# Kernel optimization log

Measured on AMD Instinct MI355X. Metric: run time of the kernel, lower is better.

## Reference

```python
import jax, jax.numpy as jnp
import numpy as np

B, S, D, H = 4, 2048, 1024, 16
HD = D // H  # head dim = 64


def setup_inputs() -> dict:
    key = jax.random.key(0)
    ks = jax.random.split(key, 6)
    scale = D ** -0.5
    x = jax.random.normal(ks[0], (B, S, D), dtype=jnp.float32)
    # per-head q/k/v projections stacked: [H, D, HD] (bias-free, as in GPT Head)
    Wq = jax.random.normal(ks[1], (H, D, HD), dtype=jnp.float32) * scale
    Wk = jax.random.normal(ks[2], (H, D, HD), dtype=jnp.float32) * scale
    Wv = jax.random.normal(ks[3], (H, D, HD), dtype=jnp.float32) * scale
    # output projection Linear(D, D) with bias
    Wp = jax.random.normal(ks[4], (D, D), dtype=jnp.float32) * scale
    bp = jax.random.normal(ks[5], (D,), dtype=jnp.float32) * 0.01
    return {"x": x, "Wq": Wq, "Wk": Wk, "Wv": Wv, "Wp": Wp, "bp": bp}


def reference(x, Wq, Wk, Wv, Wp, bp):
    # q,k,v: [B, H, S, HD]
    q = jnp.einsum("bsd,hdk->bhsk", x, Wq)
    k = jnp.einsum("bsd,hdk->bhsk", x, Wk)
    v = jnp.einsum("bsd,hdk->bhsk", x, Wv)
    scale = HD ** -0.5
    # attention scores [B, H, S, S] with causal mask
    scores = jnp.einsum("bhsk,bhtk->bhst", q, k) * scale
    causal = jnp.tril(jnp.ones((S, S), dtype=bool))
    scores = jnp.where(causal, scores, jnp.finfo(scores.dtype).min)
    att = jax.nn.softmax(scores, axis=-1)
    out = jnp.einsum("bhst,bhtk->bhsk", att, v)  # [B, H, S, HD]
    # concat heads -> [B, S, D], then output projection
    out = out.transpose(0, 2, 1, 3).reshape(B, S, D)
    return out @ Wp + bp
```

## Files before the change

kernel.cpp:

```cpp
#include <hip/hip_runtime.h>
#include <stdint.h>

#define B_  4
#define S_  2048
#define D_  1024
#define H_  16
#define HD_ 64

typedef __attribute__((ext_vector_type(8))) short bf16x8;
typedef __attribute__((ext_vector_type(4))) short bf16x4;
typedef __attribute__((ext_vector_type(4))) float f32x4;

#define MFMA32(a, b, c) __builtin_amdgcn_mfma_f32_16x16x32_bf16(a, b, c, 0, 0, 0)

__device__ __forceinline__ unsigned short f2bf(float f) {
  union { float f; uint32_t u; } cv; cv.f = f;
  uint32_t x = cv.u;
  uint32_t r = (x + 0x7fffu + ((x >> 16) & 1u)) >> 16;
  return (unsigned short)r;
}

__device__ __forceinline__ unsigned short f2bf_rz(float f) {
  union { float f; uint32_t u; } cv; cv.f = f;
  return (unsigned short)(cv.u >> 16);
}

__device__ __forceinline__ void gload_lds16(const unsigned short* g, unsigned short* l) {
  __builtin_amdgcn_global_load_lds((const __attribute__((address_space(1))) void*)g,
                                   (__attribute__((address_space(3))) void*)l, 16, 0, 0);
}

__global__ void k_cast_x(const float* __restrict__ x, unsigned short* __restrict__ xb) {
  size_t i = ((size_t)blockIdx.x * 256 + threadIdx.x) * 8;
  float4 a = *(const float4*)(x + i);
  float4 b = *(const float4*)(x + i + 4);
  bf16x8 o;
  o[0] = (short)f2bf(a.x); o[1] = (short)f2bf(a.y);
  o[2] = (short)f2bf(a.z); o[3] = (short)f2bf(a.w);
  o[4] = (short)f2bf(b.x); o[5] = (short)f2bf(b.y);
  o[6] = (short)f2bf(b.z); o[7] = (short)f2bf(b.w);
  *(bf16x8*)(xb + i) = o;
}

__global__ void k_wqkv_t(const float* __restrict__ Wq, const float* __restrict__ Wk,
                         const float* __restrict__ Wv, unsigned short* __restrict__ W1T) {
  __shared__ unsigned short tile[64][65];
  const float* W = (blockIdx.z == 0) ? Wq : (blockIdx.z == 1) ? Wk : Wv;
  int h = blockIdx.y;
  int d0 = blockIdx.x * 64;
  int tx = threadIdx.x & 63;
  int tg = threadIdx.x >> 6;
  const float* src = W + (size_t)h * (D_ * HD_) + (size_t)d0 * HD_;
#pragma unroll
  for (int r = 0; r < 16; ++r) {
    int dy = tg * 16 + r;
    tile[tx][dy] = f2bf(src[(size_t)dy * HD_ + tx]);
  }
  __syncthreads();
  unsigned short* dst = W1T + ((size_t)blockIdx.z * 1024 + (size_t)h * 64) * 1024 + d0;
#pragma unroll
  for (int r = 0; r < 16; ++r) {
    int hd = tg * 16 + r;
    dst[(size_t)hd * 1024 + tx] = tile[hd][tx];
  }
}

__global__ void k_wp_t(const float* __restrict__ Wp, unsigned short* __restrict__ WpT) {
  __shared__ unsigned short tile[64][65];
  int n0 = blockIdx.x * 64, k0 = blockIdx.y * 64;
  int tx = threadIdx.x & 63;
  int tg = threadIdx.x >> 6;
#pragma unroll
  for (int r = 0; r < 16; ++r) {
    int ky = tg * 16 + r;
    tile[tx][ky] = f2bf(Wp[(size_t)(k0 + ky) * D_ + n0 + tx]);
  }
  __syncthreads();
#pragma unroll
  for (int r = 0; r < 16; ++r) {
    int ny = tg * 16 + r;
    WpT[(size_t)(n0 + ny) * D_ + k0 + tx] = tile[ny][tx];
  }
}

__global__ __launch_bounds__(256) void k_gemm_qkv(const unsigned short* __restrict__ xb,
                                                  const unsigned short* __restrict__ W1T,
                                                  unsigned short* __restrict__ qb,
                                                  unsigned short* __restrict__ kb,
                                                  unsigned short* __restrict__ vt) {
  __shared__ __align__(16) unsigned short lds[128 * 136];
  unsigned short* As = lds;
  unsigned short* Bs = lds + 4096;
  const int K = 1024;
  int tid = threadIdx.x;
  int lane = tid & 63;
  int w = tid >> 6;
  int c = lane & 15, g = lane >> 4;
  int wr = w >> 1, wc = w & 1;
  int nwg = gridDim.x * gridDim.y;
  int bid = blockIdx.y * gridDim.x + blockIdx.x;
  int swzb = (bid & 7) * (nwg >> 3) + (bid >> 3);
  int bx = swzb % gridDim.x, by = swzb / gridDim.x;
  int m0 = by * 128;
  int n0 = bx * 128;
  f32x4 acc[4][4];
#pragma unroll
  for (int m = 0; m < 4; ++m)
#pragma unroll
    for (int n = 0; n < 4; ++n) acc[m][n] = (f32x4){0.f, 0.f, 0.f, 0.f};

  int t0 = tid, t1 = tid + 256;
  const unsigned short* ga0 = xb + (size_t)(m0 + (t0 >> 2)) * K + 8 * (t0 & 3);
  const unsigned short* ga1 = xb + (size_t)(m0 + (t1 >> 2)) * K + 8 * (t1 & 3);
  const unsigned short* gb0 = W1T + (size_t)(n0 + (t0 >> 2)) * K + 8 * (t0 & 3);
  const unsigned short* gb1 = W1T + (size_t)(n0 + (t1 >> 2)) * K + 8 * (t1 & 3);

  for (int kk = 0; kk < K; kk += 32) {
    __syncthreads();
    gload_lds16(ga0 + kk, &As[t0 * 8]);
    gload_lds16(ga1 + kk, &As[t1 * 8]);
    gload_lds16(gb0 + kk, &Bs[t0 * 8]);
    gload_lds16(gb1 + kk, &Bs[t1 * 8]);
    __syncthreads();
    bf16x8 af[4], bfr[4];
#pragma unroll
    for (int m = 0; m < 4; ++m)
      af[m] = *(const bf16x8*)&As[(wr * 64 + m * 16 + c) * 32 + 8 * g];
#pragma unroll
    for (int n = 0; n < 4; ++n)
      bfr[n] = *(const bf16x8*)&Bs[(wc * 64 + n * 16 + c) * 32 + 8 * g];
#pragma unroll
    for (int m = 0; m < 4; ++m)
#pragma unroll
      for (int n = 0; n < 4; ++n) acc[m][n] = MFMA32(af[m], bfr[n], acc[m][n]);
  }

  int qkv = n0 >> 10;
  int b = m0 >> 11;
  int s0 = m0 & 2047;
  if (qkv < 2) {
    unsigned short* dst = (qkv == 0) ? qb : kb;
    float sc = (qkv == 0) ? 0.125f : 1.0f;
#pragma unroll
    for (int m = 0; m < 4; ++m)
#pragma unroll
      for (int n = 0; n < 4; ++n)
#pragma unroll
        for (int r = 0; r < 4; ++r) {
          int s = s0 + wr * 64 + m * 16 + 4 * g + r;
          int Cn = n0 + wc * 64 + n * 16 + c;
          int h = (Cn >> 6) & 15;
          int hd = Cn & 63;
          dst[((size_t)(b * 16 + h) * S_ + s) * HD_ + hd] = f2bf(acc[m][n][r] * sc);
        }
  } else {
    __syncthreads();
#pragma unroll
    for (int m = 0; m < 4; ++m)
#pragma unroll
      for (int n = 0; n < 4; ++n) {
        int col = wc * 64 + n * 16 + c;
        int row4 = wr * 64 + m * 16 + 4 * g;
        bf16x4 pk;
        pk[0] = (short)f2bf(acc[m][n][0]);
        pk[1] = (short)f2bf(acc[m][n][1]);
        pk[2] = (short)f2bf(acc[m][n][2]);
        pk[3] = (short)f2bf(acc[m][n][3]);
        *(bf16x4*)&lds[col * 136 + row4] = pk;
      }
    __syncthreads();
    int col = tid >> 1;
    int sh = (tid & 1) * 64;
    int Cn = n0 + col;
    int h = (Cn >> 6) & 15;
    int hd = Cn & 63;
    unsigned short* dst = vt + ((size_t)(b * 16 + h) * HD_ + hd) * S_ + s0 + sh;
#pragma unroll
    for (int j = 0; j < 8; ++j)
      *(bf16x8*)(dst + 8 * j) = *(const bf16x8*)&lds[col * 136 + sh + 8 * j];
  }
}

__device__ __forceinline__ void stage_kv(const unsigned short* kp, const unsigned short* vp,
                                         int tb, unsigned short* Ks, unsigned short* Vs,
                                         int tid) {
  int i0 = tid, i1 = tid + 256;
  int r0 = i0 >> 3, ch0 = ((i0 & 7) ^ (r0 & 7)) << 3;
  int r1 = i1 >> 3, ch1 = ((i1 & 7) ^ (r1 & 7)) << 3;
  gload_lds16(kp + (size_t)(tb + r0) * HD_ + ch0, &Ks[i0 * 8]);
  gload_lds16(kp + (size_t)(tb + r1) * HD_ + ch1, &Ks[i1 * 8]);
  gload_lds16(vp + (size_t)r0 * S_ + tb + ch0, &Vs[i0 * 8]);
  gload_lds16(vp + (size_t)r1 * S_ + tb + ch1, &Vs[i1 * 8]);
}

__global__ __launch_bounds__(256) void k_attn(const unsigned short* __restrict__ qb,
                                              const unsigned short* __restrict__ kb,
                                              const unsigned short* __restrict__ vt,
                                              unsigned short* __restrict__ attn) {
  __shared__ __align__(16) unsigned short Ks[2][64 * 64];
  __shared__ __align__(16) unsigned short Vs[2][64 * 64];
  int tid = threadIdx.x;
  int lane = tid & 63;
  int w = tid >> 6;
  int c = lane & 15, g = lane >> 4;
  int swz = ((blockIdx.x & 7) << 6) | (blockIdx.x >> 3);
  int bh = swz >> 3;
  int pr = swz & 7;
  const unsigned short* kp = kb + (size_t)bh * S_ * HD_;
  const unsigned short* vp = vt + (size_t)bh * HD_ * S_;
  int b = bh >> 4, h = bh & 15;

  for (int p = 0; p < 2; ++p) {
    int j = p ? (15 - pr) : pr;
    int q0w = j * 128 + w * 32;
    const unsigned short* qp = qb + ((size_t)bh * S_ + q0w) * HD_;
    bf16x8 qf[2][2];
#pragma unroll
    for (int qs = 0; qs < 2; ++qs)
#pragma unroll
      for (int h2 = 0; h2 < 2; ++h2)
        qf[qs][h2] = *(const bf16x8*)(qp + (size_t)(qs * 16 + c) * HD_ + h2 * 32 + 8 * g);

    const f32x4 fz = {0.f, 0.f, 0.f, 0.f};
    f32x4 oacc[4][2];
#pragma unroll
    for (int c4 = 0; c4 < 4; ++c4)
#pragma unroll
      for (int qs = 0; qs < 2; ++qs) oacc[c4][qs] = fz;
    float m[2] = {-1e30f, -1e30f};
    float l[2] = {0.f, 0.f};

    int nkb = 2 * j + 2;
    int nkw = (q0w + 95) >> 6;

    stage_kv(kp, vp, 0, Ks[0], Vs[0], tid);
    __syncthreads();

    for (int kt = 0; kt < nkb; ++kt) {
      int cur = kt & 1;
      if (kt + 1 < nkb) stage_kv(kp, vp, (kt + 1) << 6, Ks[cur ^ 1], Vs[cur ^ 1], tid);
      if (kt < nkw) {
        int tb = kt << 6;
        const unsigned short* KsC = Ks[cur];
        const unsigned short* VsC = Vs[cur];
        f32x4 st[4][2];
#pragma unroll
        for (int k4 = 0; k4 < 4; ++k4) {
          int row = k4 * 16 + c;
          int rx = row & 7;
          bf16x8 a0 = *(const bf16x8*)&KsC[row * 64 + ((g ^ rx) << 3)];
          bf16x8 a1 = *(const bf16x8*)&KsC[row * 64 + (((4 + g) ^ rx) << 3)];
#pragma unroll
          for (int qs = 0; qs < 2; ++qs) {
            f32x4 t0 = MFMA32(a0, qf[qs][0], fz);
            st[k4][qs] = MFMA32(a1, qf[qs][1], t0);
          }
        }
        if (tb + 63 > q0w) {
#pragma unroll
          for (int k4 = 0; k4 < 4; ++k4)
#pragma unroll
            for (int qs = 0; qs < 2; ++qs)
#pragma unroll
              for (int r = 0; r < 4; ++r)
                if (tb + k4 * 16 + 4 * g + r > q0w + qs * 16 + c) st[k4][qs][r] = -1e30f;
        }
        bf16x8 pa[2][2];
#pragma unroll
        for (int qs = 0; qs < 2; ++qs) {
          float mx = -1e30f;
#pragma unroll
          for (int k4 = 0; k4 < 4; ++k4)
#pragma unroll
            for (int r = 0; r < 4; ++r) mx = fmaxf(mx, st[k4][qs][r]);
          mx = fmaxf(mx, __shfl_xor(mx, 16));
          mx = fmaxf(mx, __shfl_xor(mx, 32));
          if (!__all(mx - m[qs] <= 8.f)) {
            float m_new = fmaxf(m[qs], mx);
            float resc = __expf(m[qs] - m_new);
            m[qs] = m_new;
            float rb0 = __shfl(resc, 4 * g + 0);
            float rb1 = __shfl(resc, 4 * g + 1);
            float rb2 = __shfl(resc, 4 * g + 2);
            float rb3 = __shfl(resc, 4 * g + 3);
#pragma unroll
            for (int c4 = 0; c4 < 4; ++c4) {
              oacc[c4][qs][0] *= rb0; oacc[c4][qs][1] *= rb1;
              oacc[c4][qs][2] *= rb2; oacc[c4][qs][3] *= rb3;
            }
            l[qs] *= resc;
          }
          float mh = m[qs];
          float rs = 0.f;
#pragma unroll
          for (int k4 = 0; k4 < 4; ++k4)
#pragma unroll
            for (int r = 0; r < 4; ++r) {
              float e = __expf(st[k4][qs][r] - mh);
              st[k4][qs][r] = e;
              rs += e;
            }
          rs += __shfl_xor(rs, 16);
          rs += __shfl_xor(rs, 32);
          l[qs] += rs;
#pragma unroll
          for (int ks = 0; ks < 2; ++ks)
#pragma unroll
            for (int jj = 0; jj < 8; ++jj)
              pa[qs][ks][jj] = (short)f2bf_rz(st[ks * 2 + (jj >> 2)][qs][jj & 3]);
        }
#pragma unroll
        for (int c4 = 0; c4 < 4; ++c4) {
          int row = c4 * 16 + c;
          int rx = row & 7;
#pragma unroll
          for (int ks = 0; ks < 2; ++ks) {
            int e0 = ks * 32 + 4 * g;
            int e1 = e0 + 16;
            int s0 = (((e0 >> 3) ^ rx) << 3) | (e0 & 7);
            int s1 = (((e1 >> 3) ^ rx) << 3) | (e1 & 7);
            bf16x4 v0 = *(const bf16x4*)&VsC[row * 64 + s0];
            bf16x4 v1 = *(const bf16x4*)&VsC[row * 64 + s1];
            bf16x8 vf;
            vf[0] = v0[0]; vf[1] = v0[1]; vf[2] = v0[2]; vf[3] = v0[3];
            vf[4] = v1[0]; vf[5] = v1[1]; vf[6] = v1[2]; vf[7] = v1[3];
#pragma unroll
            for (int qs = 0; qs < 2; ++qs)
              oacc[c4][qs] = MFMA32(pa[qs][ks], vf, oacc[c4][qs]);
          }
        }
      }
      __syncthreads();
    }
#pragma unroll
    for (int qs = 0; qs < 2; ++qs) {
      float linv = 1.f / l[qs];
      float lb0 = __shfl(linv, 4 * g + 0);
      float lb1 = __shfl(linv, 4 * g + 1);
      float lb2 = __shfl(linv, 4 * g + 2);
      float lb3 = __shfl(linv, 4 * g + 3);
      float lb[4] = {lb0, lb1, lb2, lb3};
      unsigned short* op = attn + ((size_t)b * S_ + q0w + qs * 16) * D_ + h * HD_;
#pragma unroll
      for (int c4 = 0; c4 < 4; ++c4)
#pragma unroll
        for (int r = 0; r < 4; ++r)
          op[(size_t)(4 * g + r) * D_ + c4 * 16 + c] = f2bf(oacc[c4][qs][r] * lb[r]);
    }
  }
}

__global__ __launch_bounds__(256) void k_gemm_out(const unsigned short* __restrict__ at,
                                                  const unsigned short* __restrict__ WpT,
                                                  const float* __restrict__ bp,
                                                  float* __restrict__ out) {
  __shared__ __align__(16) unsigned short As[128 * 32];
  __shared__ __align__(16) unsigned short Bs[128 * 32];
  const int K = 1024;
  int tid = threadIdx.x;
  int lane = tid & 63;
  int w = tid >> 6;
  int c = lane & 15, g = lane >> 4;
  int wr = w >> 1, wc = w & 1;
  int nwg = gridDim.x * gridDim.y;
  int bid = blockIdx.y * gridDim.x + blockIdx.x;
  int swzb = (bid & 7) * (nwg >> 3) + (bid >> 3);
  int bx = swzb % gridDim.x, by = swzb / gridDim.x;
  int m0 = by * 128;
  int n0 = bx * 128;
  f32x4 acc[4][4];
#pragma unroll
  for (int m = 0; m < 4; ++m)
#pragma unroll
    for (int n = 0; n < 4; ++n) acc[m][n] = (f32x4){0.f, 0.f, 0.f, 0.f};

  int t0 = tid, t1 = tid + 256;
  const unsigned short* ga0 = at + (size_t)(m0 + (t0 >> 2)) * K + 8 * (t0 & 3);
  const unsigned short* ga1 = at + (size_t)(m0 + (t1 >> 2)) * K + 8 * (t1 & 3);
  const unsigned short* gb0 = WpT + (size_t)(n0 + (t0 >> 2)) * K + 8 * (t0 & 3);
  const unsigned short* gb1 = WpT + (size_t)(n0 + (t1 >> 2)) * K + 8 * (t1 & 3);

  for (int kk = 0; kk < K; kk += 32) {
    __syncthreads();
    gload_lds16(ga0 + kk, &As[t0 * 8]);
    gload_lds16(ga1 + kk, &As[t1 * 8]);
    gload_lds16(gb0 + kk, &Bs[t0 * 8]);
    gload_lds16(gb1 + kk, &Bs[t1 * 8]);
    __syncthreads();
    bf16x8 af[4], bfr[4];
#pragma unroll
    for (int m = 0; m < 4; ++m)
      af[m] = *(const bf16x8*)&As[(wr * 64 + m * 16 + c) * 32 + 8 * g];
#pragma unroll
    for (int n = 0; n < 4; ++n)
      bfr[n] = *(const bf16x8*)&Bs[(wc * 64 + n * 16 + c) * 32 + 8 * g];
#pragma unroll
    for (int m = 0; m < 4; ++m)
#pragma unroll
      for (int n = 0; n < 4; ++n) acc[m][n] = MFMA32(af[m], bfr[n], acc[m][n]);
  }

#pragma unroll
  for (int m = 0; m < 4; ++m)
#pragma unroll
    for (int n = 0; n < 4; ++n)
#pragma unroll
      for (int r = 0; r < 4; ++r) {
        int R = m0 + wr * 64 + m * 16 + 4 * g + r;
        int Cn = n0 + wc * 64 + n * 16 + c;
        out[(size_t)R * D_ + Cn] = acc[m][n][r] + bp[Cn];
      }
}

extern "C" void kernel_launch(void* const* d_in, const int* in_sizes, int n_in,
                              void* d_out, int out_size, void* d_ws, size_t ws_size,
                              hipStream_t stream) {
  const float* x  = (const float*)d_in[0];
  const float* Wq = (const float*)d_in[1];
  const float* Wk = (const float*)d_in[2];
  const float* Wv = (const float*)d_in[3];
  const float* Wp = (const float*)d_in[4];
  const float* bp = (const float*)d_in[5];
  float* out = (float*)d_out;
  char* ws = (char*)d_ws;
  unsigned short* xb  = (unsigned short*)(ws);
  unsigned short* w1t = (unsigned short*)(ws + (size_t)(16u << 20));
  unsigned short* wpt = (unsigned short*)(ws + (size_t)(22u << 20));
  unsigned short* qb  = (unsigned short*)(ws + (size_t)(24u << 20));
  unsigned short* kb  = (unsigned short*)(ws + (size_t)(40u << 20));
  unsigned short* vt  = (unsigned short*)(ws + (size_t)(56u << 20));
  unsigned short* at  = xb;

  k_cast_x<<<dim3(4096), dim3(256), 0, stream>>>(x, xb);
  k_wqkv_t<<<dim3(16, 16, 3), dim3(256), 0, stream>>>(Wq, Wk, Wv, w1t);
  k_wp_t<<<dim3(16, 16), dim3(256), 0, stream>>>(Wp, wpt);
  k_gemm_qkv<<<dim3(24, 64), dim3(256), 0, stream>>>(xb, w1t, qb, kb, vt);
  k_attn<<<dim3(512), dim3(256), 0, stream>>>(qb, kb, vt, at);
  k_gemm_out<<<dim3(8, 64), dim3(256), 0, stream>>>(at, wpt, bp, out);
}
```

Before: 191.3 us.

## Remap GEMM blocks to XCD row bands and halve QKV epilogue LDS footprint

Adds a block mapping that gives each XCD a contiguous band of M rows and walks N tiles within it, so A tiles are shared through the per-XCD L2 in both GEMMs. The V-transpose epilogue in the QKV GEMM now stages one 64-column half at a time, which shrinks the LDS array from 128x136 to 8704 elements. The goal is better cache reuse and more resident blocks per CU. The cost is an extra pair of barriers, and only half the threads do the stores in each pass.

```diff
diff --git a/kernel.cpp b/kernel.cpp
--- a/kernel.cpp
+++ b/kernel.cpp
@@ -83,12 +83,21 @@
   }
 }
 
+__device__ __forceinline__ void block_map(int& bx, int& by) {
+  int bid = blockIdx.y * gridDim.x + blockIdx.x;
+  int xcd = bid & 7;
+  int idx = bid >> 3;
+  int bandH = gridDim.y >> 3;
+  by = xcd * bandH + (idx % bandH);
+  bx = idx / bandH;
+}
+
 __global__ __launch_bounds__(256) void k_gemm_qkv(const unsigned short* __restrict__ xb,
                                                   const unsigned short* __restrict__ W1T,
                                                   unsigned short* __restrict__ qb,
                                                   unsigned short* __restrict__ kb,
                                                   unsigned short* __restrict__ vt) {
-  __shared__ __align__(16) unsigned short lds[128 * 136];
+  __shared__ __align__(16) unsigned short lds[8704];
   unsigned short* As = lds;
   unsigned short* Bs = lds + 4096;
   const int K = 1024;
@@ -97,10 +106,8 @@
   int w = tid >> 6;
   int c = lane & 15, g = lane >> 4;
   int wr = w >> 1, wc = w & 1;
-  int nwg = gridDim.x * gridDim.y;
-  int bid = blockIdx.y * gridDim.x + blockIdx.x;
-  int swzb = (bid & 7) * (nwg >> 3) + (bid >> 3);
-  int bx = swzb % gridDim.x, by = swzb / gridDim.x;
+  int bx, by;
+  block_map(bx, by);
   int m0 = by * 128;
   int n0 = bx * 128;
   f32x4 acc[4][4];
@@ -154,30 +161,37 @@
           dst[((size_t)(b * 16 + h) * S_ + s) * HD_ + hd] = f2bf(acc[m][n][r] * sc);
         }
   } else {
-    __syncthreads();
-#pragma unroll
-    for (int m = 0; m < 4; ++m)
-#pragma unroll
-      for (int n = 0; n < 4; ++n) {
-        int col = wc * 64 + n * 16 + c;
-        int row4 = wr * 64 + m * 16 + 4 * g;
-        bf16x4 pk;
-        pk[0] = (short)f2bf(acc[m][n][0]);
-        pk[1] = (short)f2bf(acc[m][n][1]);
-        pk[2] = (short)f2bf(acc[m][n][2]);
-        pk[3] = (short)f2bf(acc[m][n][3]);
-        *(bf16x4*)&lds[col * 136 + row4] = pk;
+#pragma unroll
+    for (int colh = 0; colh < 2; ++colh) {
+      __syncthreads();
+      if (wc == colh) {
+#pragma unroll
+        for (int m = 0; m < 4; ++m)
+#pragma unroll
+          for (int n = 0; n < 4; ++n) {
+            int coll = n * 16 + c;
+            int row4 = wr * 64 + m * 16 + 4 * g;
+            bf16x4 pk;
+            pk[0] = (short)f2bf(acc[m][n][0]);
+            pk[1] = (short)f2bf(acc[m][n][1]);
+            pk[2] = (short)f2bf(acc[m][n][2]);
+            pk[3] = (short)f2bf(acc[m][n][3]);
+            *(bf16x4*)&lds[coll * 136 + row4] = pk;
+          }
       }
-    __syncthreads();
-    int col = tid >> 1;
-    int sh = (tid & 1) * 64;
-    int Cn = n0 + col;
-    int h = (Cn >> 6) & 15;
-    int hd = Cn & 63;
-    unsigned short* dst = vt + ((size_t)(b * 16 + h) * HD_ + hd) * S_ + s0 + sh;
-#pragma unroll
-    for (int j = 0; j < 8; ++j)
-      *(bf16x8*)(dst + 8 * j) = *(const bf16x8*)&lds[col * 136 + sh + 8 * j];
+      __syncthreads();
+      if (tid < 128) {
+        int coll = tid >> 1;
+        int sh = (tid & 1) * 64;
+        int Cn = n0 + colh * 64 + coll;
+        int h = (Cn >> 6) & 15;
+        int hd = Cn & 63;
+        unsigned short* dst = vt + ((size_t)(b * 16 + h) * HD_ + hd) * S_ + s0 + sh;
+#pragma unroll
+        for (int j = 0; j < 8; ++j)
+          *(bf16x8*)(dst + 8 * j) = *(const bf16x8*)&lds[coll * 136 + sh + 8 * j];
+      }
+    }
   }
 }
 
@@ -362,10 +376,8 @@
   int w = tid >> 6;
   int c = lane & 15, g = lane >> 4;
   int wr = w >> 1, wc = w & 1;
-  int nwg = gridDim.x * gridDim.y;
-  int bid = blockIdx.y * gridDim.x + blockIdx.x;
-  int swzb = (bid & 7) * (nwg >> 3) + (bid >> 3);
-  int bx = swzb % gridDim.x, by = swzb / gridDim.x;
+  int bx, by;
+  block_map(bx, by);
   int m0 = by * 128;
   int n0 = bx * 128;
   f32x4 acc[4][4];
```

Result: slower. 235.4 us (+23.1%).

## Split QKV GEMM into pipelined 256x256 QK kernel and transposed V GEMM

Applied to the files above, without the earlier changes.

Replaces the single QKV projection GEMM with two kernels. The Q/K kernel uses 256x256 tiles with 512 threads, double-buffered swizzled LDS staging that is interleaved with the MFMA work, and priority hints, to raise MFMA utilisation. V is computed as a separate GEMM, W_v^T times x^T, so results come out already transposed and the LDS transpose epilogue is dropped. This adds a kernel launch, and the V kernel's epilogue now does scattered 2-byte global stores.

```diff
diff --git a/kernel.cpp b/kernel.cpp
--- a/kernel.cpp
+++ b/kernel.cpp
@@ -83,14 +83,138 @@
   }
 }
 
-__global__ __launch_bounds__(256) void k_gemm_qkv(const unsigned short* __restrict__ xb,
-                                                  const unsigned short* __restrict__ W1T,
-                                                  unsigned short* __restrict__ qb,
-                                                  unsigned short* __restrict__ kb,
-                                                  unsigned short* __restrict__ vt) {
-  __shared__ __align__(16) unsigned short lds[128 * 136];
-  unsigned short* As = lds;
-  unsigned short* Bs = lds + 4096;
+__device__ __forceinline__ void stage_half(const unsigned short* g0, unsigned short* l0, int tid) {
+  int r0 = tid >> 2, s0 = tid & 3;
+  gload_lds16(g0 + (size_t)r0 * 1024 + ((s0 ^ ((r0 >> 1) & 3)) << 3), l0 + tid * 8);
+  int r1 = r0 + 128;
+  gload_lds16(g0 + (size_t)r1 * 1024 + ((s0 ^ ((r1 >> 1) & 3)) << 3), l0 + 4096 + tid * 8);
+}
+
+__device__ __forceinline__ bf16x8 rd_swz(const unsigned short* base, int row, int g) {
+  return *(const bf16x8*)&base[row * 32 + ((g ^ ((row >> 1) & 3)) << 3)];
+}
+
+__global__ __launch_bounds__(512, 2) void k_gemm_qk(const unsigned short* __restrict__ xb,
+                                                    const unsigned short* __restrict__ W1T,
+                                                    unsigned short* __restrict__ qb,
+                                                    unsigned short* __restrict__ kb) {
+  __shared__ __align__(16) unsigned short As[32768];
+  __shared__ __align__(16) unsigned short Bs[32768];
+  int tid = threadIdx.x;
+  int lane = tid & 63;
+  int wid = tid >> 6;
+  int c = lane & 15, g = lane >> 4;
+  int wr = wid >> 2, wc = wid & 3;
+  int bid = blockIdx.x;
+  int xcd = bid & 7, idx = bid >> 3;
+  int by = (xcd << 2) | (idx & 3);
+  int bx = idx >> 2;
+  int m0 = by << 8, n0 = bx << 8;
+  const unsigned short* gA = xb + (size_t)m0 * 1024;
+  const unsigned short* gB = W1T + (size_t)n0 * 1024;
+
+  f32x4 acc[8][4];
+#pragma unroll
+  for (int i = 0; i < 8; ++i)
+#pragma unroll
+    for (int n = 0; n < 4; ++n) acc[i][n] = (f32x4){0.f, 0.f, 0.f, 0.f};
+
+  stage_half(gA + 0,  As + 0, tid);
+  stage_half(gB + 0,  Bs + 0, tid);
+  stage_half(gA + 32, As + 8192, tid);
+  stage_half(gB + 32, Bs + 8192, tid);
+
+  for (int t = 0; t < 16; ++t) {
+    int sl = (t & 1) << 14;
+    int so = sl ^ 16384;
+    int kn = (t + 1) << 6;
+    bool pf = (t < 15);
+    const unsigned short* Asl = As + sl;
+    const unsigned short* Bsl = Bs + sl;
+    bf16x8 bf[4];
+
+    asm volatile("s_waitcnt vmcnt(4)" ::: "memory");
+    __builtin_amdgcn_s_barrier();
+    if (pf) stage_half(gA + kn, As + so, tid);
+#pragma unroll
+    for (int n = 0; n < 4; ++n) bf[n] = rd_swz(Bsl, wc * 64 + n * 16 + c, g);
+    {
+      bf16x8 af[4];
+#pragma unroll
+      for (int j = 0; j < 4; ++j) af[j] = rd_swz(Asl, wr * 128 + j * 16 + c, g);
+      __builtin_amdgcn_s_setprio(1);
+#pragma unroll
+      for (int j = 0; j < 4; ++j)
+#pragma unroll
+        for (int n = 0; n < 4; ++n) acc[j][n] = MFMA32(af[j], bf[n], acc[j][n]);
+      __builtin_amdgcn_s_setprio(0);
+    }
+    if (pf) stage_half(gB + kn, Bs + so, tid);
+    {
+      bf16x8 af[4];
+#pragma unroll
+      for (int j = 0; j < 4; ++j) af[j] = rd_swz(Asl, wr * 128 + (4 + j) * 16 + c, g);
+      __builtin_amdgcn_s_setprio(1);
+#pragma unroll
+      for (int j = 0; j < 4; ++j)
+#pragma unroll
+        for (int n = 0; n < 4; ++n) acc[4 + j][n] = MFMA32(af[j], bf[n], acc[4 + j][n]);
+      __builtin_amdgcn_s_setprio(0);
+    }
+    asm volatile("s_waitcnt vmcnt(4)" ::: "memory");
+    __builtin_amdgcn_s_barrier();
+    if (pf) stage_half(gA + kn + 32, As + so + 8192, tid);
+#pragma unroll
+    for (int n = 0; n < 4; ++n) bf[n] = rd_swz(Bsl + 8192, wc * 64 + n * 16 + c, g);
+    {
+      bf16x8 af[4];
+#pragma unroll
+      for (int j = 0; j < 4; ++j) af[j] = rd_swz(Asl + 8192, wr * 128 + j * 16 + c, g);
+      __builtin_amdgcn_s_setprio(1);
+#pragma unroll
+      for (int j = 0; j < 4; ++j)
+#pragma unroll
+        for (int n = 0; n < 4; ++n) acc[j][n] = MFMA32(af[j], bf[n], acc[j][n]);
+      __builtin_amdgcn_s_setprio(0);
+    }
+    if (pf) stage_half(gB + kn + 32, Bs + so + 8192, tid);
+    {
+      bf16x8 af[4];
+#pragma unroll
+      for (int j = 0; j < 4; ++j) af[j] = rd_swz(Asl + 8192, wr * 128 + (4 + j) * 16 + c, g);
+      __builtin_amdgcn_s_setprio(1);
+#pragma unroll
+      for (int j = 0; j < 4; ++j)
+#pragma unroll
+        for (int n = 0; n < 4; ++n) acc[4 + j][n] = MFMA32(af[j], bf[n], acc[4 + j][n]);
+      __builtin_amdgcn_s_setprio(0);
+    }
+  }
+
+  int Cnb = n0 + wc * 64;
+  int qkv = Cnb >> 10;
+  int h = (Cnb >> 6) & 15;
+  int b = m0 >> 11;
+  int s0 = m0 & 2047;
+  unsigned short* dst = ((qkv == 0) ? qb : kb) + ((size_t)(b * 16 + h) * S_) * HD_;
+  float sc = (qkv == 0) ? 0.125f : 1.0f;
+#pragma unroll
+  for (int mrep = 0; mrep < 8; ++mrep)
+#pragma unroll
+    for (int n = 0; n < 4; ++n)
+#pragma unroll
+      for (int r = 0; r < 4; ++r) {
+        int s = s0 + wr * 128 + mrep * 16 + 4 * g + r;
+        int hd = n * 16 + c;
+        dst[(size_t)s * HD_ + hd] = f2bf(acc[mrep][n][r] * sc);
+      }
+}
+
+__global__ __launch_bounds__(256) void k_gemm_vt(const unsigned short* __restrict__ W1T,
+                                                 const unsigned short* __restrict__ xb,
+                                                 unsigned short* __restrict__ vt) {
+  __shared__ __align__(16) unsigned short As[128 * 32];
+  __shared__ __align__(16) unsigned short Bs[128 * 32];
   const int K = 1024;
   int tid = threadIdx.x;
   int lane = tid & 63;
@@ -103,6 +227,7 @@
   int bx = swzb % gridDim.x, by = swzb / gridDim.x;
   int m0 = by * 128;
   int n0 = bx * 128;
+  const unsigned short* Av = W1T + (size_t)2048 * 1024;
   f32x4 acc[4][4];
 #pragma unroll
   for (int m = 0; m < 4; ++m)
@@ -110,10 +235,10 @@
     for (int n = 0; n < 4; ++n) acc[m][n] = (f32x4){0.f, 0.f, 0.f, 0.f};
 
   int t0 = tid, t1 = tid + 256;
-  const unsigned short* ga0 = xb + (size_t)(m0 + (t0 >> 2)) * K + 8 * (t0 & 3);
-  const unsigned short* ga1 = xb + (size_t)(m0 + (t1 >> 2)) * K + 8 * (t1 & 3);
-  const unsigned short* gb0 = W1T + (size_t)(n0 + (t0 >> 2)) * K + 8 * (t0 & 3);
-  const unsigned short* gb1 = W1T + (size_t)(n0 + (t1 >> 2)) * K + 8 * (t1 & 3);
+  const unsigned short* ga0 = Av + (size_t)(m0 + (t0 >> 2)) * K + 8 * (t0 & 3);
+  const unsigned short* ga1 = Av + (size_t)(m0 + (t1 >> 2)) * K + 8 * (t1 & 3);
+  const unsigned short* gb0 = xb + (size_t)(n0 + (t0 >> 2)) * K + 8 * (t0 & 3);
+  const unsigned short* gb1 = xb + (size_t)(n0 + (t1 >> 2)) * K + 8 * (t1 & 3);
 
   for (int kk = 0; kk < K; kk += 32) {
     __syncthreads();
@@ -135,50 +260,18 @@
       for (int n = 0; n < 4; ++n) acc[m][n] = MFMA32(af[m], bfr[n], acc[m][n]);
   }
 
-  int qkv = n0 >> 10;
-  int b = m0 >> 11;
-  int s0 = m0 & 2047;
-  if (qkv < 2) {
-    unsigned short* dst = (qkv == 0) ? qb : kb;
-    float sc = (qkv == 0) ? 0.125f : 1.0f;
-#pragma unroll
-    for (int m = 0; m < 4; ++m)
-#pragma unroll
-      for (int n = 0; n < 4; ++n)
-#pragma unroll
-        for (int r = 0; r < 4; ++r) {
-          int s = s0 + wr * 64 + m * 16 + 4 * g + r;
-          int Cn = n0 + wc * 64 + n * 16 + c;
-          int h = (Cn >> 6) & 15;
-          int hd = Cn & 63;
-          dst[((size_t)(b * 16 + h) * S_ + s) * HD_ + hd] = f2bf(acc[m][n][r] * sc);
-        }
-  } else {
-    __syncthreads();
-#pragma unroll
-    for (int m = 0; m < 4; ++m)
-#pragma unroll
-      for (int n = 0; n < 4; ++n) {
-        int col = wc * 64 + n * 16 + c;
-        int row4 = wr * 64 + m * 16 + 4 * g;
-        bf16x4 pk;
-        pk[0] = (short)f2bf(acc[m][n][0]);
-        pk[1] = (short)f2bf(acc[m][n][1]);
-        pk[2] = (short)f2bf(acc[m][n][2]);
-        pk[3] = (short)f2bf(acc[m][n][3]);
-        *(bf16x4*)&lds[col * 136 + row4] = pk;
+  int b = (n0 >> 11);
+#pragma unroll
+  for (int m = 0; m < 4; ++m)
+#pragma unroll
+    for (int n = 0; n < 4; ++n)
+#pragma unroll
+      for (int r = 0; r < 4; ++r) {
+        int vm = m0 + wr * 64 + m * 16 + 4 * g + r;
+        int Cn = n0 + wc * 64 + n * 16 + c;
+        int s = Cn & 2047;
+        vt[((size_t)(b << 10) + vm) * S_ + s] = f2bf(acc[m][n][r]);
       }
-    __syncthreads();
-    int col = tid >> 1;
-    int sh = (tid & 1) * 64;
-    int Cn = n0 + col;
-    int h = (Cn >> 6) & 15;
-    int hd = Cn & 63;
-    unsigned short* dst = vt + ((size_t)(b * 16 + h) * HD_ + hd) * S_ + s0 + sh;
-#pragma unroll
-    for (int j = 0; j < 8; ++j)
-      *(bf16x8*)(dst + 8 * j) = *(const bf16x8*)&lds[col * 136 + sh + 8 * j];
-  }
 }
 
 __device__ __forceinline__ void stage_kv(const unsigned short* kp, const unsigned short* vp,
@@ -434,7 +527,8 @@
   k_cast_x<<<dim3(4096), dim3(256), 0, stream>>>(x, xb);
   k_wqkv_t<<<dim3(16, 16, 3), dim3(256), 0, stream>>>(Wq, Wk, Wv, w1t);
   k_wp_t<<<dim3(16, 16), dim3(256), 0, stream>>>(Wp, wpt);
-  k_gemm_qkv<<<dim3(24, 64), dim3(256), 0, stream>>>(xb, w1t, qb, kb, vt);
+  k_gemm_qk<<<dim3(256), dim3(512), 0, stream>>>(xb, w1t, qb, kb);
+  k_gemm_vt<<<dim3(64, 8), dim3(256), 0, stream>>>(w1t, xb, vt);
   k_attn<<<dim3(512), dim3(256), 0, stream>>>(qb, kb, vt, at);
   k_gemm_out<<<dim3(8, 64), dim3(256), 0, stream>>>(at, wpt, bp, out);
 }
```

Result: faster. 184.8 us (-3.4%).
